# Optimization experiments

Measured on AMD Instinct MI355X. Metric: run time of the kernel, lower is better.

## Reference

```python
import jax, jax.numpy as jnp
import numpy as np

B, S, D, H, DH = 4, 1024, 1024, 16, 64  # batch, seq, d_model, heads, head dim (d_Q=d_K=d_V)


def setup_inputs() -> dict:
    key = jax.random.key(0)
    ks = jax.random.split(key, 12)
    std = 0.02
    return {
        "x_Q": jax.random.normal(ks[0], (B, S, D), jnp.float32),
        "x_K": jax.random.normal(ks[1], (B, S, D), jnp.float32),
        "x_V": jax.random.normal(ks[2], (B, S, D), jnp.float32),
        "src_batch_lens": jax.random.randint(ks[3], (B,), 0, S),
        # stacked per-head projection weights: [H, d_model, head_dim]
        "Wq": jax.random.normal(ks[4], (H, D, DH), jnp.float32) * std,
        "bq": jax.random.normal(ks[5], (H, DH), jnp.float32) * std,
        "Wk": jax.random.normal(ks[6], (H, D, DH), jnp.float32) * std,
        "bk": jax.random.normal(ks[7], (H, DH), jnp.float32) * std,
        "Wv": jax.random.normal(ks[8], (H, D, DH), jnp.float32) * std,
        "bv": jax.random.normal(ks[9], (H, DH), jnp.float32) * std,
        "Wo": jax.random.normal(ks[10], (D, D), jnp.float32) * std,
        "bo": jax.random.normal(ks[11], (D,), jnp.float32) * std,
    }


def reference(x_Q, x_K, x_V, src_batch_lens, Wq, bq, Wk, bk, Wv, bv, Wo, bo):
    dq = Wq.shape[-1]
    seq = x_Q.shape[1]
    # all heads at once instead of the per-head python loop
    Q = jnp.einsum('bsd,hde->bhse', x_Q, Wq) + bq[None, :, None, :]
    K = jnp.einsum('bsd,hde->bhse', x_K, Wk) + bk[None, :, None, :]
    V = jnp.einsum('bsd,hde->bhse', x_V, Wv) + bv[None, :, None, :]
    scores = jnp.einsum('bhse,bhte->bhst', Q, K) / jnp.sqrt(jnp.asarray(dq, x_Q.dtype))
    # original: matmul(diag(1..1,0..0), scores) zeroes query rows >= length
    rowmask = (jnp.arange(seq)[None, :] < src_batch_lens[:, None])  # [B, S]
    scores = scores * rowmask[:, None, :, None].astype(scores.dtype)
    A = jax.nn.softmax(scores, axis=-1)  # torch Softmax(dim=2) on [B,S,S] per head = key axis
    AV = jnp.einsum('bhst,bhtv->bhsv', A, V)
    out = AV.transpose(0, 2, 1, 3).reshape(x_Q.shape[0], seq, -1)  # concat heads on dim 2
    return out @ Wo + bo  # dropout p=0 -> identity
```

## Files before the change

### kernel.cpp

```cpp
#include <hip/hip_runtime.h>
#include <stdint.h>

typedef short v8s __attribute__((ext_vector_type(8)));
typedef short v4s __attribute__((ext_vector_type(4)));
typedef float v4f __attribute__((ext_vector_type(4)));

#define AS1 __attribute__((address_space(1)))
#define AS3 __attribute__((address_space(3)))

__device__ __forceinline__ void glds16(const void* g, void* l) {
  __builtin_amdgcn_global_load_lds((const AS1 void*)g, (AS3 void*)l, 16, 0, 0);
}

__device__ __forceinline__ short f2bf(float f) {
  uint32_t u = __float_as_uint(f);
  u += 0x7fffu + ((u >> 16) & 1u);
  return (short)(u >> 16);
}

__global__ __launch_bounds__(256) void prep_kernel(
    const float* __restrict__ xQ, const float* __restrict__ xK, const float* __restrict__ xV,
    const float* __restrict__ wq, const float* __restrict__ wk, const float* __restrict__ wv,
    const float* __restrict__ wo,
    short* __restrict__ oxQ, short* __restrict__ oxK, short* __restrict__ oxV,
    short* __restrict__ oq, short* __restrict__ ok, short* __restrict__ ov,
    short* __restrict__ oo) {
  const int bid = blockIdx.x;
  const int t = threadIdx.x;
  if (bid >= 1024) {
    const int c = bid - 1024;
    const int z = c >> 12;
    const int i = (c & 4095) * 256 + t;
    const float* in = (z == 0) ? xQ : (z == 1) ? xK : xV;
    short* out      = (z == 0) ? oxQ : (z == 1) ? oxK : oxV;
    float4 v = ((const float4*)in)[i];
    short4 o = { f2bf(v.x), f2bf(v.y), f2bf(v.z), f2bf(v.w) };
    ((short4*)out)[i] = o;
    return;
  }
  __shared__ float tile[64][65];
  const float* in;
  short* out;
  int C, R, rb, cb;
  if (bid < 768) {
    const int which = bid >> 8, rem = bid & 255;
    const int slice = rem >> 4, rbi = rem & 15;
    in  = ((which == 0) ? wq : (which == 1) ? wk : wv) + (size_t)slice * 65536;
    out = ((which == 0) ? oq : (which == 1) ? ok : ov) + (size_t)slice * 65536;
    C = 64; R = 1024; rb = rbi * 64; cb = 0;
  } else {
    const int r = bid - 768;
    in = wo; out = oo;
    C = 1024; R = 1024; rb = (r >> 4) * 64; cb = (r & 15) * 64;
  }
  const int col = t & 63, r0 = t >> 6;
#pragma unroll
  for (int i = 0; i < 16; ++i) {
    int row = r0 + i * 4;
    tile[row][col] = in[(size_t)(rb + row) * C + cb + col];
  }
  __syncthreads();
#pragma unroll
  for (int i = 0; i < 16; ++i) {
    int orow = r0 + i * 4;
    out[(size_t)(cb + orow) * R + rb + col] = f2bf(tile[col][orow]);
  }
}

template <int MR>
__device__ __forceinline__ void gemm_core(const short* __restrict__ Ag,
                                          const short* __restrict__ Bg,
                                          short* As, short* Bs,
                                          v4f (&acc)[MR / 32][4]) {
  constexpr int MT = MR / 32;
  constexpr int ASZ = MR * 32;
  constexpr int BSZ = 128 * 32;
  const int tid  = threadIdx.x;
  const int lane = tid & 63;
  const int w    = tid >> 6;
  const int quad = lane >> 4;
  const int c15  = lane & 15;
  const int wr   = (w >> 1) * (MR / 2);
  const int wc   = (w & 1) * 64;

  const int r0 = tid >> 2;
  const int p0 = (tid & 3) ^ ((r0 & 3) ^ ((r0 >> 2) & 3));
  const short* a0 = Ag + (size_t)r0 * 1024 + p0 * 8;
  const short* a1 = a0 + 64 * 1024;
  const short* b0 = Bg + (size_t)r0 * 1024 + p0 * 8;
  const short* b1 = b0 + 64 * 1024;
  short* lA = As + tid * 8;
  short* lB = Bs + tid * 8;

  auto issue = [&](int t, int buf) {
    const int o = t * 32;
    glds16(a0 + o, lA + buf * ASZ);
    if constexpr (MR == 128) glds16(a1 + o, lA + buf * ASZ + 2048);
    glds16(b0 + o, lB + buf * BSZ);
    glds16(b1 + o, lB + buf * BSZ + 2048);
  };

  issue(0, 0);
  issue(1, 1);

  const int xs = (c15 & 3) ^ ((c15 >> 2) & 3);
  const int rdoff = ((quad ^ xs)) * 8;

  for (int kb = 0; kb < 32; ++kb) {
    if constexpr (MR == 128)
      asm volatile("s_waitcnt vmcnt(4)\n\ts_barrier" ::: "memory");
    else
      asm volatile("s_waitcnt vmcnt(3)\n\ts_barrier" ::: "memory");

    const int t2 = kb + 2;
    issue(t2 < 32 ? t2 : 31, t2 % 3);

    const short* Ab = As + (kb % 3) * ASZ;
    const short* Bb = Bs + (kb % 3) * BSZ;

    v8s a[MT], b[4];
#pragma unroll
    for (int mt = 0; mt < MT; ++mt)
      a[mt] = *(const v8s*)(Ab + (wr + mt * 16 + c15) * 32 + rdoff);
#pragma unroll
    for (int nt = 0; nt < 4; ++nt)
      b[nt] = *(const v8s*)(Bb + (wc + nt * 16 + c15) * 32 + rdoff);
#pragma unroll
    for (int mt = 0; mt < MT; ++mt)
#pragma unroll
      for (int nt = 0; nt < 4; ++nt)
        acc[mt][nt] = __builtin_amdgcn_mfma_f32_16x16x32_bf16(a[mt], b[nt], acc[mt][nt], 0, 0, 0);
  }
}

__global__ __launch_bounds__(256, 3) void proj_gemm(
    const short* __restrict__ xQ, const short* __restrict__ xK, const short* __restrict__ xV,
    const short* __restrict__ WqT, const short* __restrict__ WkT, const short* __restrict__ WvT,
    const float* __restrict__ bq, const float* __restrict__ bk, const float* __restrict__ bv,
    short* __restrict__ Qb, short* __restrict__ Kb, short* __restrict__ Vtb) {
  __shared__ short As[12288];
  __shared__ short Bs[12288];
  const int lin = blockIdx.x;
  const int z = lin >> 8;
  const int r = lin & 255;
  const int nb = ((r >> 3) & 7) * 128;
  const int mb = (((r & 7) << 2) + (r >> 6)) * 128;
  const short* A    = (z == 0) ? xQ  : (z == 1) ? xK  : xV;
  const short* Bt   = (z == 0) ? WqT : (z == 1) ? WkT : WvT;
  const float* bias = (z == 0) ? bq  : (z == 1) ? bk  : bv;
  short* outp       = (z == 0) ? Qb  : (z == 1) ? Kb  : Vtb;
  v4f acc[4][4] = {};
  gemm_core<128>(A + (size_t)mb * 1024, Bt + (size_t)nb * 1024, As, Bs, acc);

  const int lane = threadIdx.x & 63, w = threadIdx.x >> 6;
  const int quad = lane >> 4, c15 = lane & 15;
  const int wr = (w >> 1) * 64, wc = (w & 1) * 64;
  const bool vmode = (z == 2);
#pragma unroll
  for (int nt = 0; nt < 4; ++nt) {
    const int gn = nb + wc + nt * 16 + c15;
    const float bb = bias[gn];
    const int h = gn >> 6, e = gn & 63;
#pragma unroll
    for (int mt = 0; mt < 4; ++mt) {
      if (!vmode) {
#pragma unroll
        for (int rr = 0; rr < 4; ++rr) {
          const int gm = mb + wr + mt * 16 + quad * 4 + rr;
          const int bi = gm >> 10, s = gm & 1023;
          const size_t base = (size_t)(bi * 16 + h) * 65536;
          outp[base + (size_t)s * 64 + e] = f2bf(acc[mt][nt][rr] + bb);
        }
      } else {
        const int gm0 = mb + wr + mt * 16 + quad * 4;
        const int bi = gm0 >> 10, s0 = gm0 & 1023;
        const size_t base = (size_t)(bi * 16 + h) * 65536;
        short4 st = { f2bf(acc[mt][nt][0] + bb), f2bf(acc[mt][nt][1] + bb),
                      f2bf(acc[mt][nt][2] + bb), f2bf(acc[mt][nt][3] + bb) };
        *(short4*)&outp[base + (size_t)e * 1024 + s0] = st;
      }
    }
  }
}

__global__ __launch_bounds__(256, 3) void out_gemm(
    const short* __restrict__ AV, const short* __restrict__ WoT,
    const float* __restrict__ bo, float* __restrict__ outp) {
  __shared__ short As[6144];
  __shared__ short Bs[12288];
  const int lin = blockIdx.x;
  const int nb = ((lin >> 3) & 7) * 128;
  const int mb = (((lin & 7) << 3) + (lin >> 6)) * 64;
  v4f acc[2][4] = {};
  gemm_core<64>(AV + (size_t)mb * 1024, WoT + (size_t)nb * 1024, As, Bs, acc);
  const int lane = threadIdx.x & 63, w = threadIdx.x >> 6;
  const int quad = lane >> 4, c15 = lane & 15;
  const int wr = (w >> 1) * 32, wc = (w & 1) * 64;
#pragma unroll
  for (int nt = 0; nt < 4; ++nt) {
    const int gn = nb + wc + nt * 16 + c15;
    const float bb = bo[gn];
#pragma unroll
    for (int mt = 0; mt < 2; ++mt)
#pragma unroll
      for (int r = 0; r < 4; ++r) {
        const int gm = mb + wr + mt * 16 + quad * 4 + r;
        outp[(size_t)gm * 1024 + gn] = acc[mt][nt][r] + bb;
      }
  }
}

__global__ __launch_bounds__(256, 2) void attn_kernel(
    const short* __restrict__ Qb, const short* __restrict__ Kb,
    const short* __restrict__ Vtb, const int* __restrict__ lens,
    short* __restrict__ AVb) {
  __shared__ short Ks[2][4096];
  __shared__ short Vs[2][4096];
  const int tid = threadIdx.x, lane = tid & 63, w = tid >> 6;
  const int quad = lane >> 4, c15 = lane & 15;
  const int flat = blockIdx.x;
  const int bh = (flat & 7) + 8 * ((flat >> 3) & 7);
  const int qg = flat >> 6;
  const int b = bh >> 4, h = bh & 15;
  const short* Qp = Qb  + (size_t)bh * 65536;
  const short* Kp = Kb  + (size_t)bh * 65536;
  const short* Vp = Vtb + (size_t)bh * 65536;
  const int len = lens[b];
  const int row0 = qg * 128 + w * 32;

  v8s bq_[2][2];
#pragma unroll
  for (int qf = 0; qf < 2; ++qf)
#pragma unroll
    for (int kf = 0; kf < 2; ++kf)
      bq_[qf][kf] = *(const v8s*)(Qp + (size_t)(row0 + qf * 16 + c15) * 64 + kf * 32 + quad * 8);

  float scale[2];
  scale[0] = (row0 + c15 < len) ? 0.125f : 0.0f;
  scale[1] = (row0 + 16 + c15 < len) ? 0.125f : 0.0f;
  float sm[2] = {0.f, 0.f};
  v4f o[2][4] = {};

  const int srow = tid >> 3, spart = tid & 7;
  const int gpart = spart ^ (srow & 7);
  const int kgo0 = srow * 64 + gpart * 8, kgo1 = (srow + 32) * 64 + gpart * 8;
  const int vgo0 = srow * 1024 + gpart * 8, vgo1 = (srow + 32) * 1024 + gpart * 8;
  const int l0 = tid * 8, l1 = 2048 + tid * 8;

  const int c7 = c15 & 7;
  const int krow = c15 * 128;
  const int koff0 = krow + ((quad) ^ c7) * 16;
  const int koff1 = krow + ((4 + quad) ^ c7) * 16;
  const int q2 = quad >> 1, h8 = (quad & 1) * 8;
  int voff[4];
#pragma unroll
  for (int nt = 0; nt < 4; ++nt)
    voff[nt] = krow + ((2 * nt + q2) ^ c7) * 16 + h8;

  glds16(Kp + kgo0, (char*)Ks[0] + l0 * 2);
  glds16(Kp + kgo1, (char*)Ks[0] + l1 * 2);
  glds16(Vp + vgo0, (char*)Vs[0] + l0 * 2);
  glds16(Vp + vgo1, (char*)Vs[0] + l1 * 2);

  for (int kb = 0; kb < 16; ++kb) {
    const int cur = kb & 1, nxt = cur ^ 1;
    __syncthreads();

    if (kb < 15) {
      const short* kt = Kp + (size_t)(kb + 1) * 4096;
      const short* vt = Vp + (kb + 1) * 64;
      glds16(kt + kgo0, (char*)Ks[nxt] + l0 * 2);
      glds16(kt + kgo1, (char*)Ks[nxt] + l1 * 2);
      glds16(vt + vgo0, (char*)Vs[nxt] + l0 * 2);
      glds16(vt + vgo1, (char*)Vs[nxt] + l1 * 2);
    }

    v8s ak[4][2];
#pragma unroll
    for (int nt = 0; nt < 4; ++nt) {
      ak[nt][0] = *(const v8s*)((const char*)Ks[cur] + nt * 2048 + koff0);
      ak[nt][1] = *(const v8s*)((const char*)Ks[cur] + nt * 2048 + koff1);
    }

    v4f sc[2][4];
#pragma unroll
    for (int qf = 0; qf < 2; ++qf)
#pragma unroll
      for (int nt = 0; nt < 4; ++nt) {
        v4f z = {};
#pragma unroll
        for (int kf = 0; kf < 2; ++kf)
          z = __builtin_amdgcn_mfma_f32_16x16x32_bf16(ak[nt][kf], bq_[qf][kf], z, 0, 0, 0);
        sc[qf][nt] = z;
      }

    v4s pb[2][4];
#pragma unroll
    for (int qf = 0; qf < 2; ++qf)
#pragma unroll
      for (int nt = 0; nt < 4; ++nt) {
        v4s pv;
#pragma unroll
        for (int r = 0; r < 4; ++r) {
          float p = __expf(sc[qf][nt][r] * scale[qf]);
          sm[qf] += p;
          pv[r] = f2bf(p);
        }
        pb[qf][nt] = pv;
      }

    v4s av[4][4];
#pragma unroll
    for (int t = 0; t < 4; ++t)
#pragma unroll
      for (int nt = 0; nt < 4; ++nt)
        av[t][nt] = *(const v4s*)((const char*)Vs[cur] + t * 2048 + voff[nt]);

#pragma unroll
    for (int t = 0; t < 4; ++t)
#pragma unroll
      for (int nt = 0; nt < 4; ++nt) {
        o[0][t] = __builtin_amdgcn_mfma_f32_16x16x16bf16_1k(av[t][nt], pb[0][nt], o[0][t], 0, 0, 0);
        o[1][t] = __builtin_amdgcn_mfma_f32_16x16x16bf16_1k(av[t][nt], pb[1][nt], o[1][t], 0, 0, 0);
      }
  }

#pragma unroll
  for (int qf = 0; qf < 2; ++qf) {
    float s = sm[qf];
    s += __shfl_xor(s, 16);
    s += __shfl_xor(s, 32);
    const float inv = 1.0f / s;
    const size_t rowbase = (size_t)(b * 1024 + row0 + qf * 16 + c15) * 1024 + h * 64;
#pragma unroll
    for (int t = 0; t < 4; ++t) {
      short4 st = { f2bf(o[qf][t][0] * inv), f2bf(o[qf][t][1] * inv),
                    f2bf(o[qf][t][2] * inv), f2bf(o[qf][t][3] * inv) };
      *(short4*)&AVb[rowbase + t * 16 + quad * 4] = st;
    }
  }
}

extern "C" void kernel_launch(void* const* d_in, const int* in_sizes, int n_in,
                              void* d_out, int out_size, void* d_ws, size_t ws_size,
                              hipStream_t stream) {
  const float* xQ = (const float*)d_in[0];
  const float* xK = (const float*)d_in[1];
  const float* xV = (const float*)d_in[2];
  const int* lens = (const int*)d_in[3];
  const float* Wq = (const float*)d_in[4];
  const float* bq = (const float*)d_in[5];
  const float* Wk = (const float*)d_in[6];
  const float* bk = (const float*)d_in[7];
  const float* Wv = (const float*)d_in[8];
  const float* bv = (const float*)d_in[9];
  const float* Wo = (const float*)d_in[10];
  const float* bo = (const float*)d_in[11];
  float* out = (float*)d_out;

  char* ws = (char*)d_ws;
  short* xQb = (short*)(ws + 0);
  short* xKb = (short*)(ws + 8388608);
  short* xVb = (short*)(ws + 16777216);
  short* WqT = (short*)(ws + 25165824);
  short* WkT = (short*)(ws + 27262976);
  short* WvT = (short*)(ws + 29360128);
  short* WoT = (short*)(ws + 31457280);
  short* Qb  = (short*)(ws + 33554432);
  short* Kb  = (short*)(ws + 41943040);
  short* Vtb = (short*)(ws + 50331648);
  short* AVb = (short*)(ws + 58720256);

  prep_kernel<<<dim3(13312), 256, 0, stream>>>(xQ, xK, xV, Wq, Wk, Wv, Wo,
                                               xQb, xKb, xVb, WqT, WkT, WvT, WoT);
  proj_gemm<<<dim3(768), 256, 0, stream>>>(xQb, xKb, xVb, WqT, WkT, WvT,
                                           bq, bk, bv, Qb, Kb, Vtb);
  attn_kernel<<<dim3(512), 256, 0, stream>>>(Qb, Kb, Vtb, lens, AVb);
  out_gemm<<<dim3(512), 256, 0, stream>>>(AVb, WoT, bo, out);
}
```

Measured before the change: 203.2 us.

## Load GEMM B operand directly from global into registers instead of LDS

The shared GEMM core now keeps only the A tile in LDS (triple-buffered via global_load_lds) and loads each wave's B fragments straight from global memory into registers, double-buffered two K-steps ahead. The goal is to halve LDS traffic and footprint, dropping the B LDS writes and ds_reads and possibly allowing more occupancy. The cost is that B rows are now read redundantly by the two wave rows, with less coalesced global loads and more VGPR pressure. The wait counts are retuned to match the larger number of outstanding loads.

```diff
diff --git a/kernel.cpp b/kernel.cpp
--- a/kernel.cpp
+++ b/kernel.cpp
@@ -17,6 +17,8 @@
   u += 0x7fffu + ((u >> 16) & 1u);
   return (short)(u >> 16);
 }
+
+#define MFMA16(A, B, C) __builtin_amdgcn_mfma_f32_16x16x32_bf16(A, B, C, 0, 0, 0)
 
 __global__ __launch_bounds__(256) void prep_kernel(
     const float* __restrict__ xQ, const float* __restrict__ xK, const float* __restrict__ xV,
@@ -70,11 +72,10 @@
 template <int MR>
 __device__ __forceinline__ void gemm_core(const short* __restrict__ Ag,
                                           const short* __restrict__ Bg,
-                                          short* As, short* Bs,
+                                          short* As,
                                           v4f (&acc)[MR / 32][4]) {
   constexpr int MT = MR / 32;
   constexpr int ASZ = MR * 32;
-  constexpr int BSZ = 128 * 32;
   const int tid  = threadIdx.x;
   const int lane = tid & 63;
   const int w    = tid >> 6;
@@ -87,50 +88,71 @@
   const int p0 = (tid & 3) ^ ((r0 & 3) ^ ((r0 >> 2) & 3));
   const short* a0 = Ag + (size_t)r0 * 1024 + p0 * 8;
   const short* a1 = a0 + 64 * 1024;
-  const short* b0 = Bg + (size_t)r0 * 1024 + p0 * 8;
-  const short* b1 = b0 + 64 * 1024;
   short* lA = As + tid * 8;
-  short* lB = Bs + tid * 8;
-
-  auto issue = [&](int t, int buf) {
+
+  auto issueA = [&](int t, int buf) {
     const int o = t * 32;
     glds16(a0 + o, lA + buf * ASZ);
     if constexpr (MR == 128) glds16(a1 + o, lA + buf * ASZ + 2048);
-    glds16(b0 + o, lB + buf * BSZ);
-    glds16(b1 + o, lB + buf * BSZ + 2048);
   };
 
-  issue(0, 0);
-  issue(1, 1);
+  const short* Bw = Bg + (size_t)(wc + c15) * 1024 + quad * 8;
+  auto loadB = [&](v8s (&bb)[4], int t) {
+    const int o = t * 32;
+#pragma unroll
+    for (int nt = 0; nt < 4; ++nt)
+      bb[nt] = *(const v8s*)(Bw + nt * 16384 + o);
+  };
+
+  auto waitbar = [] {
+    if constexpr (MR == 128)
+      asm volatile("s_waitcnt vmcnt(6)\n\ts_barrier" ::: "memory");
+    else
+      asm volatile("s_waitcnt vmcnt(5)\n\ts_barrier" ::: "memory");
+  };
 
   const int xs = (c15 & 3) ^ ((c15 >> 2) & 3);
   const int rdoff = ((quad ^ xs)) * 8;
 
-  for (int kb = 0; kb < 32; ++kb) {
-    if constexpr (MR == 128)
-      asm volatile("s_waitcnt vmcnt(4)\n\ts_barrier" ::: "memory");
-    else
-      asm volatile("s_waitcnt vmcnt(3)\n\ts_barrier" ::: "memory");
-
-    const int t2 = kb + 2;
-    issue(t2 < 32 ? t2 : 31, t2 % 3);
-
+  auto compute = [&](int kb, v8s (&bb)[4]) {
     const short* Ab = As + (kb % 3) * ASZ;
-    const short* Bb = Bs + (kb % 3) * BSZ;
-
-    v8s a[MT], b[4];
+    v8s a[MT];
 #pragma unroll
     for (int mt = 0; mt < MT; ++mt)
       a[mt] = *(const v8s*)(Ab + (wr + mt * 16 + c15) * 32 + rdoff);
 #pragma unroll
-    for (int nt = 0; nt < 4; ++nt)
-      b[nt] = *(const v8s*)(Bb + (wc + nt * 16 + c15) * 32 + rdoff);
-#pragma unroll
     for (int mt = 0; mt < MT; ++mt)
 #pragma unroll
       for (int nt = 0; nt < 4; ++nt)
-        acc[mt][nt] = __builtin_amdgcn_mfma_f32_16x16x32_bf16(a[mt], b[nt], acc[mt][nt], 0, 0, 0);
-  }
+        acc[mt][nt] = MFMA16(a[mt], bb[nt], acc[mt][nt]);
+  };
+
+  v8s bA[4], bB[4];
+  issueA(0, 0); issueA(1, 1);
+  loadB(bA, 0); loadB(bB, 1);
+
+  asm volatile("s_waitcnt vmcnt(4)\n\ts_barrier" ::: "memory");
+  issueA(2, 2);
+  compute(0, bA);
+  loadB(bA, 2);
+
+  for (int p = 0; p < 15; ++p) {
+    const int kb = 2 * p + 1;
+    waitbar();
+    issueA(kb + 2, (kb + 2) % 3);
+    compute(kb, bB);
+    loadB(bB, kb + 2);
+    const int k2 = kb + 1;
+    waitbar();
+    {
+      const int tn = (k2 + 2 < 32) ? k2 + 2 : 31;
+      issueA(tn, (k2 + 2) % 3);
+      compute(k2, bA);
+      loadB(bA, tn);
+    }
+  }
+  waitbar();
+  compute(31, bB);
 }
 
 __global__ __launch_bounds__(256, 3) void proj_gemm(
@@ -139,7 +161,6 @@
     const float* __restrict__ bq, const float* __restrict__ bk, const float* __restrict__ bv,
     short* __restrict__ Qb, short* __restrict__ Kb, short* __restrict__ Vtb) {
   __shared__ short As[12288];
-  __shared__ short Bs[12288];
   const int lin = blockIdx.x;
   const int z = lin >> 8;
   const int r = lin & 255;
@@ -150,7 +171,7 @@
   const float* bias = (z == 0) ? bq  : (z == 1) ? bk  : bv;
   short* outp       = (z == 0) ? Qb  : (z == 1) ? Kb  : Vtb;
   v4f acc[4][4] = {};
-  gemm_core<128>(A + (size_t)mb * 1024, Bt + (size_t)nb * 1024, As, Bs, acc);
+  gemm_core<128>(A + (size_t)mb * 1024, Bt + (size_t)nb * 1024, As, acc);
 
   const int lane = threadIdx.x & 63, w = threadIdx.x >> 6;
   const int quad = lane >> 4, c15 = lane & 15;
@@ -187,12 +208,11 @@
     const short* __restrict__ AV, const short* __restrict__ WoT,
     const float* __restrict__ bo, float* __restrict__ outp) {
   __shared__ short As[6144];
-  __shared__ short Bs[12288];
   const int lin = blockIdx.x;
   const int nb = ((lin >> 3) & 7) * 128;
   const int mb = (((lin & 7) << 3) + (lin >> 6)) * 64;
   v4f acc[2][4] = {};
-  gemm_core<64>(AV + (size_t)mb * 1024, WoT + (size_t)nb * 1024, As, Bs, acc);
+  gemm_core<64>(AV + (size_t)mb * 1024, WoT + (size_t)nb * 1024, As, acc);
   const int lane = threadIdx.x & 63, w = threadIdx.x >> 6;
   const int quad = lane >> 4, c15 = lane & 15;
   const int wr = (w >> 1) * 32, wc = (w & 1) * 64;
```

Result: slower. 242.8 us (+19.5%).

## Triple-buffer K/V tiles in attention with partial vmcnt waits

Applied to the files above, without the earlier changes.

Expands the attention kernel's K/V shared-memory staging from double to triple buffering, issuing loads two tiles ahead. Each iteration waits only for the oldest outstanding loads (vmcnt(4)) before a raw barrier, so more global-to-LDS traffic overlaps with MFMA compute. This raises LDS per block from 32KB to 48KB, which may limit occupancy under the 2-blocks-per-CU launch bound. It also relies on hand-written waitcnt and barrier asm being correct with respect to how the compiler orders the memory operations.

```diff
diff --git a/kernel.cpp b/kernel.cpp
--- a/kernel.cpp
+++ b/kernel.cpp
@@ -214,8 +214,8 @@
     const short* __restrict__ Qb, const short* __restrict__ Kb,
     const short* __restrict__ Vtb, const int* __restrict__ lens,
     short* __restrict__ AVb) {
-  __shared__ short Ks[2][4096];
-  __shared__ short Vs[2][4096];
+  __shared__ short Ks[3][4096];
+  __shared__ short Vs[3][4096];
   const int tid = threadIdx.x, lane = tid & 63, w = tid >> 6;
   const int quad = lane >> 4, c15 = lane & 15;
   const int flat = blockIdx.x;
@@ -257,31 +257,26 @@
   for (int nt = 0; nt < 4; ++nt)
     voff[nt] = krow + ((2 * nt + q2) ^ c7) * 16 + h8;
 
-  glds16(Kp + kgo0, (char*)Ks[0] + l0 * 2);
-  glds16(Kp + kgo1, (char*)Ks[0] + l1 * 2);
-  glds16(Vp + vgo0, (char*)Vs[0] + l0 * 2);
-  glds16(Vp + vgo1, (char*)Vs[0] + l1 * 2);
-
-  for (int kb = 0; kb < 16; ++kb) {
-    const int cur = kb & 1, nxt = cur ^ 1;
-    __syncthreads();
-
-    if (kb < 15) {
-      const short* kt = Kp + (size_t)(kb + 1) * 4096;
-      const short* vt = Vp + (kb + 1) * 64;
-      glds16(kt + kgo0, (char*)Ks[nxt] + l0 * 2);
-      glds16(kt + kgo1, (char*)Ks[nxt] + l1 * 2);
-      glds16(vt + vgo0, (char*)Vs[nxt] + l0 * 2);
-      glds16(vt + vgo1, (char*)Vs[nxt] + l1 * 2);
+  auto issue = [&](int t) {
+    const short* kt = Kp + (size_t)t * 4096;
+    const short* vt = Vp + t * 64;
+    char* kd = (char*)Ks[t % 3];
+    char* vd = (char*)Vs[t % 3];
+    glds16(kt + kgo0, kd + l0 * 2);
+    glds16(kt + kgo1, kd + l1 * 2);
+    glds16(vt + vgo0, vd + l0 * 2);
+    glds16(vt + vgo1, vd + l1 * 2);
+  };
+
+  auto compute = [&](int kb) {
+    const char* kc = (const char*)Ks[kb % 3];
+    const char* vc = (const char*)Vs[kb % 3];
+    v8s ak[4][2];
+#pragma unroll
+    for (int nt = 0; nt < 4; ++nt) {
+      ak[nt][0] = *(const v8s*)(kc + nt * 2048 + koff0);
+      ak[nt][1] = *(const v8s*)(kc + nt * 2048 + koff1);
     }
-
-    v8s ak[4][2];
-#pragma unroll
-    for (int nt = 0; nt < 4; ++nt) {
-      ak[nt][0] = *(const v8s*)((const char*)Ks[cur] + nt * 2048 + koff0);
-      ak[nt][1] = *(const v8s*)((const char*)Ks[cur] + nt * 2048 + koff1);
-    }
-
     v4f sc[2][4];
 #pragma unroll
     for (int qf = 0; qf < 2; ++qf)
@@ -293,7 +288,6 @@
           z = __builtin_amdgcn_mfma_f32_16x16x32_bf16(ak[nt][kf], bq_[qf][kf], z, 0, 0, 0);
         sc[qf][nt] = z;
       }
-
     v4s pb[2][4];
 #pragma unroll
     for (int qf = 0; qf < 2; ++qf)
@@ -308,14 +302,12 @@
         }
         pb[qf][nt] = pv;
       }
-
     v4s av[4][4];
 #pragma unroll
     for (int t = 0; t < 4; ++t)
 #pragma unroll
       for (int nt = 0; nt < 4; ++nt)
-        av[t][nt] = *(const v4s*)((const char*)Vs[cur] + t * 2048 + voff[nt]);
-
+        av[t][nt] = *(const v4s*)(vc + t * 2048 + voff[nt]);
 #pragma unroll
     for (int t = 0; t < 4; ++t)
 #pragma unroll
@@ -323,7 +315,18 @@
         o[0][t] = __builtin_amdgcn_mfma_f32_16x16x16bf16_1k(av[t][nt], pb[0][nt], o[0][t], 0, 0, 0);
         o[1][t] = __builtin_amdgcn_mfma_f32_16x16x16bf16_1k(av[t][nt], pb[1][nt], o[1][t], 0, 0, 0);
       }
-  }
+  };
+
+  issue(0);
+  issue(1);
+
+  for (int kb = 0; kb < 15; ++kb) {
+    asm volatile("s_waitcnt vmcnt(4)\n\ts_barrier" ::: "memory");
+    if (kb <= 13) issue(kb + 2);
+    compute(kb);
+  }
+  asm volatile("s_waitcnt vmcnt(0)\n\ts_barrier" ::: "memory");
+  compute(15);
 
 #pragma unroll
   for (int qf = 0; qf < 2; ++qf) {
```

Measured after the change: 203.5 us (median of 2 runs). No clear change (+0.1%).
